# Optimization experiments

Measured on AMD Instinct MI355X. Metric: run time of the kernel, lower is better.

Reference implementation:

```python
import jax, jax.numpy as jnp
import numpy as np

IM_MAX = 1.0
IM_SIZE = 128
N_THRESHOLDS = 64


def _thresholds():
    # end = im_size * sqrt(2) // 2  (float32 math, floor-div) -> 90.0
    end = np.float32(np.float32(IM_SIZE) * np.sqrt(np.float32(2.0))) // np.float32(2.0)
    t = np.linspace(2.0, float(end), N_THRESHOLDS, dtype=np.float32)
    return np.round(t).astype(np.int32)  # half-to-even, matches torch.round


def _masks():
    # stack of circular low-pass masks, one per threshold: [T, H, W]
    crow, ccol = IM_SIZE // 2, IM_SIZE // 2
    y = np.arange(IM_SIZE)[:, None]
    x = np.arange(IM_SIZE)[None, :]
    r2 = (x - ccol) ** 2 + (y - crow) ** 2  # [H, W]
    thr = _thresholds().astype(np.int64)
    m = (r2[None, :, :] <= (thr[:, None, None] ** 2)).astype(np.float32)
    return jnp.asarray(m)


def setup_inputs() -> dict:
    key = jax.random.key(0)
    k1, k2 = jax.random.split(key)
    shape = (256, 3, IM_SIZE, IM_SIZE)
    prediction = jax.random.uniform(k1, shape, dtype=jnp.float32)
    gt = jax.random.uniform(k2, shape, dtype=jnp.float32)
    return {"prediction": prediction, "gt": gt}


def reference(prediction, gt):
    # Single FFT pass on each input (original redundantly recomputes per threshold,
    # but mask is 0/1 so masked-diff energy = mask * |pred_f - gt_f|^2).
    pf = jnp.fft.fftshift(jnp.fft.fft2(prediction), axes=(-2, -1))  # [B,C,H,W] c64
    gf = jnp.fft.fftshift(jnp.fft.fft2(gt), axes=(-2, -1))
    diff = pf - gf
    sq_err = diff.real ** 2 + diff.imag ** 2  # |.|^2, [B,C,H,W] f32
    masks = _masks()  # [T,H,W]
    # sum_sq_error per (batch, threshold): sum over C,H,W with mask
    sum_sq = jnp.einsum('thw,bchw->bt', masks, sq_err)  # [B,T]
    n_pixels = IM_SIZE * IM_SIZE
    const = 20.0 * jnp.log10(jnp.float32(IM_MAX * n_pixels))
    cf_psnr = const - 10.0 * jnp.log10(sum_sq)
    return cf_psnr
```

## Files before the change

### kernel.cpp

```cpp
#include <hip/hip_runtime.h>
#include <hip/hip_fp16.h>

#define IMG 128
#define NPIX (IMG * IMG)
#define NT 64
#define LSU 129
#define ZN (64 * LSU)

__device__ __constant__ int c_thr[NT] = {
    2, 3, 5, 6, 8, 9, 10, 12, 13, 15, 16, 17, 19, 20, 22, 23,
    24, 26, 27, 29, 30, 31, 33, 34, 36, 37, 38, 40, 41, 43, 44, 45,
    47, 48, 49, 51, 52, 54, 55, 56, 58, 59, 61, 62, 63, 65, 66, 68,
    69, 70, 72, 73, 75, 76, 77, 79, 80, 82, 83, 84, 86, 87, 89, 90};

__device__ __forceinline__ int rev7(int x) { return (int)(__brev((unsigned)x) >> 25); }

__device__ __forceinline__ unsigned packh2(float x, float y) {
    __half2 h = __floats2half2_rn(x, y);
    return *reinterpret_cast<unsigned*>(&h);
}
__device__ __forceinline__ float2 unpackh2(unsigned u) {
    __half2 h;
    *reinterpret_cast<unsigned*>(&h) = u;
    return __half22float2(h);
}

__device__ __forceinline__ float x1f(float v) {
    return __int_as_float(__builtin_amdgcn_mov_dpp(__float_as_int(v), 0xB1, 0xF, 0xF, true));
}
__device__ __forceinline__ float x2f(float v) {
    return __int_as_float(__builtin_amdgcn_mov_dpp(__float_as_int(v), 0x4E, 0xF, 0xF, true));
}
__device__ __forceinline__ float x3f(float v) {
    return __int_as_float(__builtin_amdgcn_mov_dpp(__float_as_int(v), 0x1B, 0xF, 0xF, true));
}
__device__ __forceinline__ float x7f(float v) {
    return __int_as_float(__builtin_amdgcn_mov_dpp(__float_as_int(v), 0x141, 0xF, 0xF, true));
}
__device__ __forceinline__ float x4f(float v) { return x7f(x3f(v)); }
__device__ __forceinline__ float x8f(float v) {
    return __int_as_float(__builtin_amdgcn_mov_dpp(__float_as_int(v), 0x128, 0xF, 0xF, true));
}


#define BFLY(ar, ai, br, bi, wc, wsn)              \
    do {                                           \
        const float dr_ = (ar) - (br);             \
        const float di_ = (ai) - (bi);             \
        (ar) += (br);                              \
        (ai) += (bi);                              \
        (br) = dr_ * (wc)-di_ * (wsn);             \
        (bi) = dr_ * (wsn) + di_ * (wc);           \
    } while (0)

#define XSTAGE(vr, vi, XF, cc, ss, sg)                                   \
    do {                                                                 \
        _Pragma("unroll") for (int j = 0; j < 8; ++j) {                  \
            const float pr_ = XF(vr[j]), pi_ = XF(vi[j]);                \
            const float xr_ = fmaf((sg), vr[j], pr_);                    \
            const float xi_ = fmaf((sg), vi[j], pi_);                    \
            vr[j] = xr_ * (cc)-xi_ * (ss);                               \
            vi[j] = xr_ * (ss) + xi_ * (cc);                             \
        }                                                                \
    } while (0)

#define FFT128(vr, vi)                                                            \
    do {                                                                          \
        _Pragma("unroll") for (int j = 0; j < 4; ++j)                             \
            BFLY(vr[j], vi[j], vr[j + 4], vi[j + 4], c64[j], s64[j]);             \
        BFLY(vr[0], vi[0], vr[2], vi[2], c32[0], s32[0]);                         \
        BFLY(vr[1], vi[1], vr[3], vi[3], c32[1], s32[1]);                         \
        BFLY(vr[4], vi[4], vr[6], vi[6], c32[0], s32[0]);                         \
        BFLY(vr[5], vi[5], vr[7], vi[7], c32[1], s32[1]);                         \
        _Pragma("unroll") for (int j = 0; j < 8; j += 2)                          \
            BFLY(vr[j], vi[j], vr[j + 1], vi[j + 1], c16v, s16v);                 \
        XSTAGE(vr, vi, x8f, c8v, s8v, sg8);                                       \
        XSTAGE(vr, vi, x4f, c4v, s4v, sg4);                                       \
        XSTAGE(vr, vi, x2f, c2v, s2v, sg2);                                       \
        _Pragma("unroll") for (int j = 0; j < 8; ++j) {                           \
            const float pr_ = x1f(vr[j]), pi_ = x1f(vi[j]);                       \
            vr[j] = fmaf(sg1, vr[j], pr_);                                        \
            vi[j] = fmaf(sg1, vi[j], pi_);                                        \
        }                                                                         \
    } while (0)

#define LDROW(ch, buf)                                                              \
    do {                                                                            \
        const float* pe_ = pred + ibase + (size_t)(ch)*NPIX + (size_t)(2 * rrow) * IMG; \
        const float* ge_ = gt + ibase + (size_t)(ch)*NPIX + (size_t)(2 * rrow) * IMG;   \
        _Pragma("unroll") for (int j = 0; j < 8; ++j) {                             \
            const int o_ = 16 * j + l;                                              \
            buf[j] = pe_[o_];                                                       \
            buf[8 + j] = pe_[IMG + o_];                                             \
            buf[16 + j] = ge_[o_];                                                  \
            buf[24 + j] = ge_[IMG + o_];                                            \
        }                                                                           \
    } while (0)

#define STROW(buf, zb)                                                       \
    do {                                                                     \
        _Pragma("unroll") for (int j = 0; j < 8; ++j) {                      \
            vr[j] = 0.5f * (buf[j] - buf[16 + j]);                           \
            vi[j] = 0.5f * (buf[8 + j] - buf[24 + j]);                       \
        }                                                                    \
        FFT128(vr, vi);                                                      \
        _Pragma("unroll") for (int j = 0; j < 8; ++j)                        \
            (zb)[rrow * LSU + 16 * j + l] = packh2(vr[j], vi[j]);            \
    } while (0)

#define COLONE(u, wf, zb)                                                         \
    do {                                                                          \
        const int c1_ = rev7(u);                                                  \
        const int c2_ = rev7((128 - (u)) & 127);                                  \
        _Pragma("unroll") for (int j = 0; j < 8; ++j) {                           \
            const int rowo_ = (8 * j + zr) * LSU;                                 \
            const float2 A_ = unpackh2((zb)[rowo_ + c1_]);                        \
            const float2 B_ = unpackh2((zb)[rowo_ + c2_]);                        \
            vr[j] = odd ? (A_.y + B_.y) : (A_.x + B_.x);                          \
            vi[j] = odd ? (B_.x - A_.x) : (A_.y - B_.y);                          \
        }                                                                         \
        FFT128(vr, vi);                                                           \
        const float u2f_ = (float)((u) * (u));                                    \
        _Pragma("unroll") for (int j = 0; j < 8; ++j) {                           \
            const float r2f_ = dy2f[j] + u2f_;                                    \
            if ((wf) != 0.0f && r2f_ <= 8100.0f) {                                \
                const int rc_ = (int)ceilf(sqrtf(r2f_) - 3e-4f);                  \
                atomicAdd(&s_h[wave][s_rc2bin[rc_]],                              \
                          (wf) * (vr[j] * vr[j] + vi[j] * vi[j]));                \
            }                                                                     \
        }                                                                         \
    } while (0)

#define COLPHASE(ch, zb)                                              \
    do {                                                              \
        COLONE(u0, (u0 == 0) ? 1.0f : 2.0f, zb);                      \
        if (wave == (ch)) { COLONE(64, (g == 0) ? 1.0f : 0.0f, zb); } \
    } while (0)

__global__ __launch_bounds__(1024, 4) void fused_psnr_kernel(const float* __restrict__ pred,
                                                             const float* __restrict__ gt,
                                                             float* __restrict__ out) {
    __shared__ unsigned s_z[2][ZN];
    __shared__ float s_h[16][66];
    __shared__ int s_rc2bin[91];

    const int tid = threadIdx.x;
    const int lane = tid & 63;
    const int wave = tid >> 6;
    const int l = lane & 15;
    const int g = lane >> 4;
    const int b = blockIdx.x;

    for (int i = tid; i < 16 * 66; i += 1024) (&s_h[0][0])[i] = 0.0f;
    if (tid < 91) {
        int t = 0;
        while (t < 63 && c_thr[t] < tid) ++t;
        s_rc2bin[tid] = t;
    }

    const float K = -6.2831853071795864769f * (1.0f / 128.0f);
    float c64[4], s64[4], c32[2], s32[2], c16v, s16v;
#pragma unroll
    for (int j = 0; j < 4; ++j) sincosf(K * (float)(16 * j + l), &s64[j], &c64[j]);
    sincosf(K * (float)(2 * l), &s32[0], &c32[0]);
    sincosf(K * (float)(2 * l + 32), &s32[1], &c32[1]);
    sincosf(K * (float)(4 * l), &s16v, &c16v);
    float c8v, s8v, c4v, s4v, c2v, s2v;
    sincosf(K * (float)((l & 8) ? (l & 7) * 8 : 0), &s8v, &c8v);
    sincosf(K * (float)((l & 4) ? (l & 3) * 16 : 0), &s4v, &c4v);
    sincosf(K * (float)((l & 2) ? (l & 1) * 32 : 0), &s2v, &c2v);
    const float sg8 = (l & 8) ? -1.0f : 1.0f;
    const float sg4 = (l & 4) ? -1.0f : 1.0f;
    const float sg2 = (l & 2) ? -1.0f : 1.0f;
    const float sg1 = (l & 1) ? -1.0f : 1.0f;

    const size_t ibase = (size_t)b * 3 * NPIX;
    const int rrow = (wave & 7) + 32 * (wave >> 3) + 8 * g;
    const int u0 = (wave & 3) + ((wave >> 2) << 4) + 4 * g;
    const int zr = l >> 1;
    const int odd = l & 1;

    float dy2f[8];
    const int r4 = ((l & 1) << 3) | ((l & 2) << 1) | ((l & 4) >> 1) | ((l & 8) >> 3);
#pragma unroll
    for (int j = 0; j < 8; ++j) {
        const int fy = (((j & 1) << 2) | (j & 2) | ((j & 4) >> 2)) | (r4 << 3);
        const int dy = (fy < 64) ? fy : 128 - fy;
        dy2f[j] = (float)(dy * dy);
    }

    float bufA[32], bufB[32], vr[8], vi[8];

    LDROW(0, bufA);
    STROW(bufA, s_z[0]);
    __syncthreads();

    LDROW(1, bufB);
    COLPHASE(0, s_z[0]);
    STROW(bufB, s_z[1]);
    __syncthreads();

    LDROW(2, bufA);
    COLPHASE(1, s_z[1]);
    STROW(bufA, s_z[0]);
    __syncthreads();

    COLPHASE(2, s_z[0]);
    __syncthreads();

    if (tid < 64) {
        float tot = 0.0f;
#pragma unroll
        for (int w = 0; w < 16; ++w) tot += s_h[w][tid];
        s_h[0][tid] = tot;
        float cum = 0.0f;
        for (int j = 0; j <= tid; ++j) cum += s_h[0][j];
        out[b * NT + tid] = 84.2883987849f - 10.0f * log10f(cum);
    }
}

extern "C" void kernel_launch(void* const* d_in, const int* in_sizes, int n_in,
                              void* d_out, int out_size, void* d_ws, size_t ws_size,
                              hipStream_t stream) {
    const float* pred = (const float*)d_in[0];
    const float* gt = (const float*)d_in[1];
    float* out = (float*)d_out;
    fused_psnr_kernel<<<256, 1024, 0, stream>>>(pred, gt, out);
}
```

Before: 53.75 us.

## Split work into per-channel blocks with atomic accumulation and separate PSNR pass

Instead of one 1024-thread block per batch item processing three channels in a pipelined loop, launch one 512-thread block per (batch, channel). Each block accumulates its histogram into global memory with atomics, and a third small kernel computes the cumulative PSNR. This raises the block count and occupancy and removes the double-buffered cross-channel pipeline. In exchange it adds two extra kernel launches, a zeroing pass and global atomics.

```diff
diff --git a/kernel.cpp b/kernel.cpp
--- a/kernel.cpp
+++ b/kernel.cpp
@@ -43,105 +43,103 @@
 }
 
 
-#define BFLY(ar, ai, br, bi, wc, wsn)              \
-    do {                                           \
-        const float dr_ = (ar) - (br);             \
-        const float di_ = (ai) - (bi);             \
-        (ar) += (br);                              \
-        (ai) += (bi);                              \
-        (br) = dr_ * (wc)-di_ * (wsn);             \
-        (bi) = dr_ * (wsn) + di_ * (wc);           \
-    } while (0)
-
-#define XSTAGE(vr, vi, XF, cc, ss, sg)                                   \
-    do {                                                                 \
-        _Pragma("unroll") for (int j = 0; j < 8; ++j) {                  \
-            const float pr_ = XF(vr[j]), pi_ = XF(vi[j]);                \
-            const float xr_ = fmaf((sg), vr[j], pr_);                    \
-            const float xi_ = fmaf((sg), vi[j], pi_);                    \
-            vr[j] = xr_ * (cc)-xi_ * (ss);                               \
-            vi[j] = xr_ * (ss) + xi_ * (cc);                             \
-        }                                                                \
-    } while (0)
-
-#define FFT128(vr, vi)                                                            \
-    do {                                                                          \
-        _Pragma("unroll") for (int j = 0; j < 4; ++j)                             \
-            BFLY(vr[j], vi[j], vr[j + 4], vi[j + 4], c64[j], s64[j]);             \
-        BFLY(vr[0], vi[0], vr[2], vi[2], c32[0], s32[0]);                         \
-        BFLY(vr[1], vi[1], vr[3], vi[3], c32[1], s32[1]);                         \
-        BFLY(vr[4], vi[4], vr[6], vi[6], c32[0], s32[0]);                         \
-        BFLY(vr[5], vi[5], vr[7], vi[7], c32[1], s32[1]);                         \
-        _Pragma("unroll") for (int j = 0; j < 8; j += 2)                          \
-            BFLY(vr[j], vi[j], vr[j + 1], vi[j + 1], c16v, s16v);                 \
-        XSTAGE(vr, vi, x8f, c8v, s8v, sg8);                                       \
-        XSTAGE(vr, vi, x4f, c4v, s4v, sg4);                                       \
-        XSTAGE(vr, vi, x2f, c2v, s2v, sg2);                                       \
-        _Pragma("unroll") for (int j = 0; j < 8; ++j) {                           \
-            const float pr_ = x1f(vr[j]), pi_ = x1f(vi[j]);                       \
-            vr[j] = fmaf(sg1, vr[j], pr_);                                        \
-            vi[j] = fmaf(sg1, vi[j], pi_);                                        \
-        }                                                                         \
-    } while (0)
-
-#define LDROW(ch, buf)                                                              \
-    do {                                                                            \
-        const float* pe_ = pred + ibase + (size_t)(ch)*NPIX + (size_t)(2 * rrow) * IMG; \
-        const float* ge_ = gt + ibase + (size_t)(ch)*NPIX + (size_t)(2 * rrow) * IMG;   \
-        _Pragma("unroll") for (int j = 0; j < 8; ++j) {                             \
-            const int o_ = 16 * j + l;                                              \
-            buf[j] = pe_[o_];                                                       \
-            buf[8 + j] = pe_[IMG + o_];                                             \
-            buf[16 + j] = ge_[o_];                                                  \
-            buf[24 + j] = ge_[IMG + o_];                                            \
-        }                                                                           \
-    } while (0)
-
-#define STROW(buf, zb)                                                       \
-    do {                                                                     \
-        _Pragma("unroll") for (int j = 0; j < 8; ++j) {                      \
-            vr[j] = 0.5f * (buf[j] - buf[16 + j]);                           \
-            vi[j] = 0.5f * (buf[8 + j] - buf[24 + j]);                       \
-        }                                                                    \
-        FFT128(vr, vi);                                                      \
-        _Pragma("unroll") for (int j = 0; j < 8; ++j)                        \
-            (zb)[rrow * LSU + 16 * j + l] = packh2(vr[j], vi[j]);            \
-    } while (0)
-
-#define COLONE(u, wf, zb)                                                         \
-    do {                                                                          \
-        const int c1_ = rev7(u);                                                  \
-        const int c2_ = rev7((128 - (u)) & 127);                                  \
-        _Pragma("unroll") for (int j = 0; j < 8; ++j) {                           \
-            const int rowo_ = (8 * j + zr) * LSU;                                 \
-            const float2 A_ = unpackh2((zb)[rowo_ + c1_]);                        \
-            const float2 B_ = unpackh2((zb)[rowo_ + c2_]);                        \
-            vr[j] = odd ? (A_.y + B_.y) : (A_.x + B_.x);                          \
-            vi[j] = odd ? (B_.x - A_.x) : (A_.y - B_.y);                          \
-        }                                                                         \
-        FFT128(vr, vi);                                                           \
-        const float u2f_ = (float)((u) * (u));                                    \
-        _Pragma("unroll") for (int j = 0; j < 8; ++j) {                           \
-            const float r2f_ = dy2f[j] + u2f_;                                    \
-            if ((wf) != 0.0f && r2f_ <= 8100.0f) {                                \
-                const int rc_ = (int)ceilf(sqrtf(r2f_) - 3e-4f);                  \
-                atomicAdd(&s_h[wave][s_rc2bin[rc_]],                              \
-                          (wf) * (vr[j] * vr[j] + vi[j] * vi[j]));                \
-            }                                                                     \
-        }                                                                         \
-    } while (0)
-
-#define COLPHASE(ch, zb)                                              \
+#define BFLY(ar, ai, br, bi, wc, wsn)    \
+    do {                                 \
+        const float dr_ = (ar) - (br);   \
+        const float di_ = (ai) - (bi);   \
+        (ar) += (br);                    \
+        (ai) += (bi);                    \
+        (br) = dr_ * (wc)-di_ * (wsn);   \
+        (bi) = dr_ * (wsn) + di_ * (wc); \
+    } while (0)
+
+#define XSTAGE(vr, vi, XF, cc, ss, sg)                  \
+    do {                                                \
+        _Pragma("unroll") for (int j = 0; j < 8; ++j) { \
+            const float pr_ = XF(vr[j]), pi_ = XF(vi[j]); \
+            const float xr_ = fmaf((sg), vr[j], pr_);   \
+            const float xi_ = fmaf((sg), vi[j], pi_);   \
+            vr[j] = xr_ * (cc)-xi_ * (ss);              \
+            vi[j] = xr_ * (ss) + xi_ * (cc);            \
+        }                                               \
+    } while (0)
+
+#define FFT128(vr, vi)                                                \
     do {                                                              \
-        COLONE(u0, (u0 == 0) ? 1.0f : 2.0f, zb);                      \
-        if (wave == (ch)) { COLONE(64, (g == 0) ? 1.0f : 0.0f, zb); } \
-    } while (0)
-
-__global__ __launch_bounds__(1024, 4) void fused_psnr_kernel(const float* __restrict__ pred,
-                                                             const float* __restrict__ gt,
-                                                             float* __restrict__ out) {
-    __shared__ unsigned s_z[2][ZN];
-    __shared__ float s_h[16][66];
+        _Pragma("unroll") for (int j = 0; j < 4; ++j)                 \
+            BFLY(vr[j], vi[j], vr[j + 4], vi[j + 4], c64[j], s64[j]); \
+        BFLY(vr[0], vi[0], vr[2], vi[2], c32[0], s32[0]);             \
+        BFLY(vr[1], vi[1], vr[3], vi[3], c32[1], s32[1]);             \
+        BFLY(vr[4], vi[4], vr[6], vi[6], c32[0], s32[0]);             \
+        BFLY(vr[5], vi[5], vr[7], vi[7], c32[1], s32[1]);             \
+        _Pragma("unroll") for (int j = 0; j < 8; j += 2)              \
+            BFLY(vr[j], vi[j], vr[j + 1], vi[j + 1], c16v, s16v);     \
+        XSTAGE(vr, vi, x8f, c8v, s8v, sg8);                           \
+        XSTAGE(vr, vi, x4f, c4v, s4v, sg4);                           \
+        XSTAGE(vr, vi, x2f, c2v, s2v, sg2);                           \
+        _Pragma("unroll") for (int j = 0; j < 8; ++j) {               \
+            const float pr_ = x1f(vr[j]), pi_ = x1f(vi[j]);           \
+            vr[j] = fmaf(sg1, vr[j], pr_);                            \
+            vi[j] = fmaf(sg1, vi[j], pi_);                            \
+        }                                                             \
+    } while (0)
+
+#define LDROW(rr, buf)                                                 \
+    do {                                                               \
+        const float* pe_ = pred + base + (size_t)(2 * (rr)) * IMG;     \
+        const float* ge_ = gt + base + (size_t)(2 * (rr)) * IMG;       \
+        _Pragma("unroll") for (int j = 0; j < 8; ++j) {                \
+            const int o_ = 16 * j + l;                                 \
+            buf[j] = pe_[o_];                                          \
+            buf[8 + j] = pe_[IMG + o_];                                \
+            buf[16 + j] = ge_[o_];                                     \
+            buf[24 + j] = ge_[IMG + o_];                               \
+        }                                                              \
+    } while (0)
+
+#define STROW(rr, buf)                                            \
+    do {                                                          \
+        _Pragma("unroll") for (int j = 0; j < 8; ++j) {           \
+            vr[j] = 0.5f * (buf[j] - buf[16 + j]);                \
+            vi[j] = 0.5f * (buf[8 + j] - buf[24 + j]);            \
+        }                                                         \
+        FFT128(vr, vi);                                           \
+        _Pragma("unroll") for (int j = 0; j < 8; ++j)             \
+            s_z[(rr)*LSU + 16 * j + l] = packh2(vr[j], vi[j]);    \
+    } while (0)
+
+#define COLONE(u, wf)                                                   \
+    do {                                                                \
+        const int c1_ = rev7(u);                                        \
+        const int c2_ = rev7((128 - (u)) & 127);                        \
+        _Pragma("unroll") for (int j = 0; j < 8; ++j) {                 \
+            const int rowo_ = (8 * j + zr) * LSU;                       \
+            const float2 A_ = unpackh2(s_z[rowo_ + c1_]);               \
+            const float2 B_ = unpackh2(s_z[rowo_ + c2_]);               \
+            vr[j] = odd ? (A_.y + B_.y) : (A_.x + B_.x);                \
+            vi[j] = odd ? (B_.x - A_.x) : (A_.y - B_.y);                \
+        }                                                               \
+        FFT128(vr, vi);                                                 \
+        const float u2f_ = (float)((u) * (u));                          \
+        _Pragma("unroll") for (int j = 0; j < 8; ++j) {                 \
+            const float r2f_ = dy2f[j] + u2f_;                          \
+            if (r2f_ <= 8100.0f) {                                      \
+                const int rc_ = (int)ceilf(sqrtf(r2f_) - 3e-4f);        \
+                atomicAdd(&s_h[wave][s_rc2bin[rc_]],                    \
+                          (wf) * (vr[j] * vr[j] + vi[j] * vi[j]));      \
+            }                                                           \
+        }                                                               \
+    } while (0)
+
+__global__ void zero_out_kernel(float* __restrict__ p) {
+    p[blockIdx.x * 256 + threadIdx.x] = 0.0f;
+}
+
+__global__ __launch_bounds__(512, 6) void fft_hist_kernel(const float* __restrict__ pred,
+                                                          const float* __restrict__ gt,
+                                                          float* __restrict__ acc) {
+    __shared__ unsigned s_z[ZN];
+    __shared__ float s_h[8][66];
     __shared__ int s_rc2bin[91];
 
     const int tid = threadIdx.x;
@@ -149,9 +147,11 @@
     const int wave = tid >> 6;
     const int l = lane & 15;
     const int g = lane >> 4;
-    const int b = blockIdx.x;
-
-    for (int i = tid; i < 16 * 66; i += 1024) (&s_h[0][0])[i] = 0.0f;
+    const int U = wave * 4 + g;
+    const int bc = blockIdx.x;
+    const int b = bc / 3;
+
+    for (int i = tid; i < 8 * 66; i += 512) (&s_h[0][0])[i] = 0.0f;
     if (tid < 91) {
         int t = 0;
         while (t < 63 && c_thr[t] < tid) ++t;
@@ -174,9 +174,7 @@
     const float sg2 = (l & 2) ? -1.0f : 1.0f;
     const float sg1 = (l & 1) ? -1.0f : 1.0f;
 
-    const size_t ibase = (size_t)b * 3 * NPIX;
-    const int rrow = (wave & 7) + 32 * (wave >> 3) + 8 * g;
-    const int u0 = (wave & 3) + ((wave >> 2) << 4) + 4 * g;
+    const size_t base = (size_t)bc * NPIX;
     const int zr = l >> 1;
     const int odd = l & 1;
 
@@ -189,34 +187,35 @@
         dy2f[j] = (float)(dy * dy);
     }
 
-    float bufA[32], bufB[32], vr[8], vi[8];
-
-    LDROW(0, bufA);
-    STROW(bufA, s_z[0]);
+    float buf[32], vr[8], vi[8];
+
+    LDROW(U, buf);
+    STROW(U, buf);
+    LDROW(U + 32, buf);
+    STROW(U + 32, buf);
     __syncthreads();
 
-    LDROW(1, bufB);
-    COLPHASE(0, s_z[0]);
-    STROW(bufB, s_z[1]);
-    __syncthreads();
-
-    LDROW(2, bufA);
-    COLPHASE(1, s_z[1]);
-    STROW(bufA, s_z[0]);
-    __syncthreads();
-
-    COLPHASE(2, s_z[0]);
+    COLONE(U, (U == 0) ? 1.0f : 2.0f);
+    COLONE(U + 32, 2.0f);
+    if (U == 0) COLONE(64, 1.0f);
     __syncthreads();
 
     if (tid < 64) {
         float tot = 0.0f;
 #pragma unroll
-        for (int w = 0; w < 16; ++w) tot += s_h[w][tid];
-        s_h[0][tid] = tot;
-        float cum = 0.0f;
-        for (int j = 0; j <= tid; ++j) cum += s_h[0][j];
-        out[b * NT + tid] = 84.2883987849f - 10.0f * log10f(cum);
+        for (int w = 0; w < 8; ++w) tot += s_h[w][tid];
+        atomicAdd(&acc[b * NT + tid], tot);
     }
+}
+
+__global__ void psnr_kernel(float* __restrict__ acc) {
+    __shared__ float h[NT];
+    const int b = blockIdx.x, t = threadIdx.x;
+    h[t] = acc[b * NT + t];
+    __syncthreads();
+    float cum = 0.0f;
+    for (int j = 0; j <= t; ++j) cum += h[j];
+    acc[b * NT + t] = 84.2883987849f - 10.0f * log10f(cum);
 }
 
 extern "C" void kernel_launch(void* const* d_in, const int* in_sizes, int n_in,
@@ -225,5 +224,8 @@
     const float* pred = (const float*)d_in[0];
     const float* gt = (const float*)d_in[1];
     float* out = (float*)d_out;
-    fused_psnr_kernel<<<256, 1024, 0, stream>>>(pred, gt, out);
-}
+
+    zero_out_kernel<<<64, 256, 0, stream>>>(out);
+    fft_hist_kernel<<<256 * 3, 512, 0, stream>>>(pred, gt, out);
+    psnr_kernel<<<256, NT, 0, stream>>>(out);
+}
```

New measurement: 61.46 us. 1.14x slower.
